# Performance work log

Hardware: AMD Instinct MI355X
Metric: run time of the kernel (lower is better)

The kernel has to match this reference:

```python
import jax, jax.numpy as jnp
import numpy as np

SCALE = 1.0          # hwcfg['scale']
MODE = 'bipolar'     # hwcfg['mode']
THRESHOLD = 0.05     # hwcfg['threshold']

T = 256              # number of stochastic-computing cycles (bit-stream length)
N = 524288           # number of independent bit streams (flattened source tensor)


def setup_inputs() -> dict:
    key = jax.random.key(0)
    k1, k2 = jax.random.split(key)
    source = jax.random.normal(k1, (N,), dtype=jnp.float32)
    # one bit per stream per cycle, values in {0, 1}
    bits = jax.random.randint(k2, (T, N), 0, 2, dtype=jnp.int32)
    return {"source": source, "bits": bits}


def reference(source, bits):
    # ProgError.__init__: clamp scaled source to [-1, 1]
    src = jnp.clip(source / SCALE, -1.0, 1.0)            # [N]

    b = bits.astype(jnp.float32)                          # [T, N]
    t = jnp.arange(1, T + 1, dtype=jnp.float32)[:, None]  # [T, 1] cycle counter

    # fused Monitor() loop: running one-count -> progressive precision per cycle
    one_cnt = jnp.cumsum(b, axis=0)                       # [T, N]
    pp = one_cnt / t                                      # [T, N]
    if MODE == 'bipolar':
        pp = pp * 2.0 - 1.0
    pe = pp - src[None, :]                                # progressive error, [T, N]

    # cycle_to_stable is overwritten with t whenever |pe| > threshold,
    # so its final value is the LAST unstable cycle (0 if never unstable)
    unstable = jnp.abs(pe) > THRESHOLD                    # [T, N] bool
    cycle_to_stable = jnp.max(jnp.where(unstable, t, 0.0), axis=0)  # [N]

    # Stability.forward(): 1 - clamp(cts, 1, T) / T
    T_f = jnp.float32(T)
    stability = 1.0 - jnp.clip(cycle_to_stable, 1.0, T_f) / T_f
    return stability
```

## Files before the change

kernel.cpp:

```cpp
#include <hip/hip_runtime.h>


#define THR 0.05f

__global__ __launch_bounds__(256) void stability_kernel(
    const float4* __restrict__ src4,
    const int4*  __restrict__ bits,
    float4* __restrict__ out4,
    int n4, int T)
{
    int i = blockIdx.x * blockDim.x + threadIdx.x;
    if (i >= n4) return;

    float4 s = src4[i];
    float s0 = fminf(fmaxf(s.x, -1.0f), 1.0f);
    float s1 = fminf(fmaxf(s.y, -1.0f), 1.0f);
    float s2 = fminf(fmaxf(s.z, -1.0f), 1.0f);
    float s3 = fminf(fmaxf(s.w, -1.0f), 1.0f);

    int c0 = 0, c1 = 0, c2 = 0, c3 = 0;
    int l0 = 0, l1 = 0, l2 = 0, l3 = 0;

    const int4* p = bits + i;
    #pragma unroll 8
    for (int t = 1; t <= T; ++t) {
        int4 b = *p;
        p += n4;
        c0 += b.x; c1 += b.y; c2 += b.z; c3 += b.w;
        float tf = (float)t;
        float pe0 = (float)c0 / tf * 2.0f - 1.0f - s0;
        float pe1 = (float)c1 / tf * 2.0f - 1.0f - s1;
        float pe2 = (float)c2 / tf * 2.0f - 1.0f - s2;
        float pe3 = (float)c3 / tf * 2.0f - 1.0f - s3;
        if (fabsf(pe0) > THR) l0 = t;
        if (fabsf(pe1) > THR) l1 = t;
        if (fabsf(pe2) > THR) l2 = t;
        if (fabsf(pe3) > THR) l3 = t;
    }

    float Tf = (float)T;
    float4 o;
    o.x = 1.0f - (float)min(max(l0, 1), T) / Tf;
    o.y = 1.0f - (float)min(max(l1, 1), T) / Tf;
    o.z = 1.0f - (float)min(max(l2, 1), T) / Tf;
    o.w = 1.0f - (float)min(max(l3, 1), T) / Tf;
    out4[i] = o;
}

extern "C" void kernel_launch(void* const* d_in, const int* in_sizes, int n_in,
                              void* d_out, int out_size, void* d_ws, size_t ws_size,
                              hipStream_t stream) {
    const float* source = (const float*)d_in[0];
    const int*   bits   = (const int*)d_in[1];
    float*       out    = (float*)d_out;

    int n  = in_sizes[0];
    int T  = in_sizes[1] / n;
    int n4 = n / 4;

    const int block = 256;
    int grid = (n4 + block - 1) / block;

    stability_kernel<<<grid, block, 0, stream>>>(
        (const float4*)source, (const int4*)bits, (float4*)out, n4, T);
}
```

Measured before the change: 717.7 us.

## Use one stream per thread with shared double reciprocal table

Changes the mapping from four streams per thread using int4 loads to one stream per thread using scalar loads, which quadruples the grid and raises occupancy. The per-cycle float division is replaced by multiplying by a double-precision reciprocal 1/t read from a shared-memory table. The launch-bounds hint now asks for 8 blocks per unit. Each thread now makes narrower loads, and the shared reciprocal table has a hard size of 256, so any T above 256 would index past it.

```diff
diff --git a/kernel.cpp b/kernel.cpp
--- a/kernel.cpp
+++ b/kernel.cpp
@@ -3,48 +3,37 @@
 
 #define THR 0.05f
 
-__global__ __launch_bounds__(256) void stability_kernel(
-    const float4* __restrict__ src4,
-    const int4*  __restrict__ bits,
-    float4* __restrict__ out4,
-    int n4, int T)
+__global__ __launch_bounds__(256, 8) void stability_kernel(
+    const float* __restrict__ src,
+    const int*   __restrict__ bits,
+    float* __restrict__ out,
+    int n, int T)
 {
-    int i = blockIdx.x * blockDim.x + threadIdx.x;
-    if (i >= n4) return;
+    __shared__ double rcp[256];
+    for (int u = threadIdx.x; u < T; u += 256)
+        rcp[u] = 1.0 / (double)(u + 1);
+    __syncthreads();
 
-    float4 s = src4[i];
-    float s0 = fminf(fmaxf(s.x, -1.0f), 1.0f);
-    float s1 = fminf(fmaxf(s.y, -1.0f), 1.0f);
-    float s2 = fminf(fmaxf(s.z, -1.0f), 1.0f);
-    float s3 = fminf(fmaxf(s.w, -1.0f), 1.0f);
+    int i = blockIdx.x * 256 + threadIdx.x;
+    if (i >= n) return;
 
-    int c0 = 0, c1 = 0, c2 = 0, c3 = 0;
-    int l0 = 0, l1 = 0, l2 = 0, l3 = 0;
+    float s = fminf(fmaxf(src[i], -1.0f), 1.0f);
 
-    const int4* p = bits + i;
+    int c = 0;
+    int l = 0;
+
+    const int* p = bits + i;
     #pragma unroll 8
-    for (int t = 1; t <= T; ++t) {
-        int4 b = *p;
-        p += n4;
-        c0 += b.x; c1 += b.y; c2 += b.z; c3 += b.w;
-        float tf = (float)t;
-        float pe0 = (float)c0 / tf * 2.0f - 1.0f - s0;
-        float pe1 = (float)c1 / tf * 2.0f - 1.0f - s1;
-        float pe2 = (float)c2 / tf * 2.0f - 1.0f - s2;
-        float pe3 = (float)c3 / tf * 2.0f - 1.0f - s3;
-        if (fabsf(pe0) > THR) l0 = t;
-        if (fabsf(pe1) > THR) l1 = t;
-        if (fabsf(pe2) > THR) l2 = t;
-        if (fabsf(pe3) > THR) l3 = t;
+    for (int t = 0; t < T; ++t) {
+        int b = *p;
+        p += n;
+        c += b;
+        float q  = (float)((double)c * rcp[t]);
+        float pe = fmaf(q, 2.0f, -1.0f) - s;
+        if (fabsf(pe) > THR) l = t + 1;
     }
 
-    float Tf = (float)T;
-    float4 o;
-    o.x = 1.0f - (float)min(max(l0, 1), T) / Tf;
-    o.y = 1.0f - (float)min(max(l1, 1), T) / Tf;
-    o.z = 1.0f - (float)min(max(l2, 1), T) / Tf;
-    o.w = 1.0f - (float)min(max(l3, 1), T) / Tf;
-    out4[i] = o;
+    out[i] = 1.0f - (float)min(max(l, 1), T) / (float)T;
 }
 
 extern "C" void kernel_launch(void* const* d_in, const int* in_sizes, int n_in,
@@ -54,13 +43,11 @@
     const int*   bits   = (const int*)d_in[1];
     float*       out    = (float*)d_out;
 
-    int n  = in_sizes[0];
-    int T  = in_sizes[1] / n;
-    int n4 = n / 4;
+    int n = in_sizes[0];
+    int T = in_sizes[1] / n;
 
     const int block = 256;
-    int grid = (n4 + block - 1) / block;
+    int grid = (n + block - 1) / block;
 
-    stability_kernel<<<grid, block, 0, stream>>>(
-        (const float4*)source, (const int4*)bits, (float4*)out, n4, T);
+    stability_kernel<<<grid, block, 0, stream>>>(source, bits, out, n, T);
 }
```

Result: faster. 677.3 us (-5.6%).
